# Optimization experiments

Measured on AMD Instinct MI355X. Metric: run time of the kernel, lower is better.

## Reference

```python
import jax, jax.numpy as jnp
import numpy as np

EMBED_DIM = 2048
NUM_HEADS = 16
HEAD_DIM = EMBED_DIM // NUM_HEADS
ROPE_BASE = 10000.0


def _rope_cos_sin(seq_len, head_dim, dtype):
    # half-split (LLaMA-style) rotary embedding tables, shape [S, D]
    inv_freq = 1.0 / (ROPE_BASE ** (jnp.arange(0, head_dim, 2, dtype=jnp.float32) / head_dim))
    ang = jnp.arange(seq_len, dtype=jnp.float32)[:, None] * inv_freq[None, :]  # [S, D/2]
    cos = jnp.concatenate([jnp.cos(ang), jnp.cos(ang)], axis=-1).astype(dtype)
    sin = jnp.concatenate([jnp.sin(ang), jnp.sin(ang)], axis=-1).astype(dtype)
    return cos, sin


def _rotate_half(t):
    d = t.shape[-1] // 2
    return jnp.concatenate([-t[..., d:], t[..., :d]], axis=-1)


def setup_inputs() -> dict:
    key = jax.random.key(0)
    ks = jax.random.split(key, 9)
    B, S, E = 2, 2048, EMBED_DIM
    sc = 1.0 / np.sqrt(E)
    return {
        "x": jax.random.normal(ks[0], (B, S, E), jnp.float32),
        "Wq": jax.random.normal(ks[1], (E, E), jnp.float32) * sc,
        "bq": jax.random.normal(ks[2], (E,), jnp.float32) * 0.01,
        "Wk": jax.random.normal(ks[3], (E, E), jnp.float32) * sc,
        "bk": jax.random.normal(ks[4], (E,), jnp.float32) * 0.01,
        "Wv": jax.random.normal(ks[5], (E, E), jnp.float32) * sc,
        "bv": jax.random.normal(ks[6], (E,), jnp.float32) * 0.01,
        "Wo": jax.random.normal(ks[7], (E, E), jnp.float32) * sc,
        "bo": jax.random.normal(ks[8], (E,), jnp.float32) * 0.01,
    }


def reference(x, Wq, bq, Wk, bk, Wv, bv, Wo, bo):
    B, S, E = x.shape
    H, D = NUM_HEADS, HEAD_DIM

    def split_heads(t):  # [B,S,E] -> [B,H,S,D]
        return t.reshape(B, S, H, D).transpose(0, 2, 1, 3)

    # torch nn.Linear: y = x @ W^T + b
    q = split_heads(x @ Wq.T + bq)
    k = split_heads(x @ Wk.T + bk)
    v = split_heads(x @ Wv.T + bv)

    cos, sin = _rope_cos_sin(S, D, x.dtype)  # [S, D]
    q = q * cos + _rotate_half(q) * sin
    k = k * cos + _rotate_half(k) * sin

    scale = 1.0 / jnp.sqrt(jnp.asarray(D, x.dtype))
    scores = jnp.einsum("bhsd,bhtd->bhst", q, k) * scale  # [B,H,S,S]
    attn = jax.nn.softmax(scores, axis=-1)
    ctx = jnp.einsum("bhst,bhtd->bhsd", attn, v)  # [B,H,S,D]
    ctx = ctx.transpose(0, 2, 1, 3).reshape(B, S, E)
    return ctx @ Wo.T + bo
```

## Files before the change

kernel.cpp:

```cpp
#include <hip/hip_runtime.h>
#include <stdint.h>

typedef unsigned short u16;
typedef unsigned int u32;
typedef __bf16 bf16x8 __attribute__((ext_vector_type(8)));
typedef u16 u16x8 __attribute__((ext_vector_type(8)));
typedef float f32x4 __attribute__((ext_vector_type(4)));
typedef float f32x16 __attribute__((ext_vector_type(16)));

#define NB 2
#define NS 2048
#define NE 2048
#define NH 16
#define ND 128
#define NM (NB*NS)

__device__ __forceinline__ float bf2f(u16 u){
  union { unsigned u; float f; } v; v.u = ((unsigned)u) << 16; return v.f;
}
__device__ __forceinline__ u16 f2bf(float f){
  union { float f; unsigned u; } v; v.f = f;
  unsigned r = v.u + 0x7fffu + ((v.u >> 16) & 1u);
  return (u16)(r >> 16);
}
__device__ __forceinline__ void gl_lds16(const u16* g, u16* l){
  __builtin_amdgcn_global_load_lds((const __attribute__((address_space(1))) unsigned int*)g,
                                   (__attribute__((address_space(3))) unsigned int*)l, 16, 0, 0);
}

__global__ __launch_bounds__(256) void k_cvt(const float* __restrict__ in, u16* __restrict__ out, int n4){
  int i = blockIdx.x * 256 + threadIdx.x;
  int stride = gridDim.x * 256;
  for (; i < n4; i += stride){
    float4 v = ((const float4*)in)[i];
    ushort4 o;
    o.x = f2bf(v.x); o.y = f2bf(v.y); o.z = f2bf(v.z); o.w = f2bf(v.w);
    ((ushort4*)out)[i] = o;
  }
}

__global__ __launch_bounds__(256) void k_cvt4(const float* __restrict__ w0, const float* __restrict__ w1,
                                              const float* __restrict__ w2, const float* __restrict__ w3,
                                              u16* __restrict__ o0, u16* __restrict__ o1,
                                              u16* __restrict__ o2, u16* __restrict__ o3){
  const int n4 = NE * NE / 4;
  int i = blockIdx.x * 256 + threadIdx.x;
  int stride = gridDim.x * 256;
  for (; i < 4 * n4; i += stride){
    int seg = i >> 20;
    int off = i & (n4 - 1);
    const float* in = seg == 0 ? w0 : seg == 1 ? w1 : seg == 2 ? w2 : w3;
    u16*        out = seg == 0 ? o0 : seg == 1 ? o1 : seg == 2 ? o2 : o3;
    float4 v = ((const float4*)in)[off];
    ushort4 o;
    o.x = f2bf(v.x); o.y = f2bf(v.y); o.z = f2bf(v.z); o.w = f2bf(v.w);
    ((ushort4*)out)[off] = o;
  }
}

__global__ __launch_bounds__(256) void k_tables(float* __restrict__ cosT, float* __restrict__ sinT){
  int idx = blockIdx.x * 256 + threadIdx.x;
  int s = idx >> 6, i = idx & 63;
  float inv = exp2f(-(float)(2 * i) * (13.287712379549449f / 128.0f));
  float ang = (float)s * inv;
  float c = cosf(ang), sn = sinf(ang);
  cosT[s * ND + i]      = c;  cosT[s * ND + 64 + i] = c;
  sinT[s * ND + i]      = sn; sinT[s * ND + 64 + i] = sn;
}

template<int MODE>
__global__ __launch_bounds__(512, 2) void k_gemm(const u16* __restrict__ A, const u16* __restrict__ W,
                                                 const float* __restrict__ bias,
                                                 const float* __restrict__ cosT, const float* __restrict__ sinT,
                                                 float qs, void* __restrict__ outp)
{
  __shared__ __align__(16) u16 lds[49152];
  const int t    = threadIdx.x;
  const int lane = t & 63;
  const int g    = lane >> 4;
  const int q    = lane & 15;
  const int wid  = t >> 6;
  const int wr   = (wid >> 1) * 64;
  const int wc   = (wid & 1) * 64;

  const int bid = blockIdx.x;
  const int v   = (bid & 7) * 32 + (bid >> 3);
  const int bm  = (v >> 4) * 256;
  const int bn  = (v & 15) * 128;

  int aoff[4], aldso[4], boff[2], bldso[2];
  #pragma unroll
  for (int c = 0; c < 4; ++c){
    int o = c * 8192 + t * 16;
    int row = o >> 7;
    int cb = (o & 127) ^ ((row & 7) << 4);
    aldso[c] = o >> 1;
    aoff[c]  = row * NE + (cb >> 1);
  }
  #pragma unroll
  for (int c = 0; c < 2; ++c){
    int o = c * 8192 + t * 16;
    int row = o >> 7;
    int cb = (o & 127) ^ ((row & 7) << 4);
    bldso[c] = o >> 1;
    boff[c]  = row * NE + (cb >> 1);
  }
  const u16* Abase = A + (size_t)bm * NE;
  const u16* Wbase = W + (size_t)bn * NE;

  int ard[2][4], brd[2][4];
  #pragma unroll
  for (int kk = 0; kk < 2; ++kk){
    #pragma unroll
    for (int m = 0; m < 4; ++m){
      int row = wr + m * 16 + q;
      ard[kk][m] = row * 128 + ((kk * 64 + g * 16) ^ ((row & 7) << 4));
    }
    #pragma unroll
    for (int n = 0; n < 4; ++n){
      int row = wc + n * 16 + q;
      brd[kk][n] = row * 128 + ((kk * 64 + g * 16) ^ ((row & 7) << 4));
    }
  }

  #pragma unroll
  for (int c = 0; c < 4; ++c) gl_lds16(Abase + aoff[c], lds + aldso[c]);
  #pragma unroll
  for (int c = 0; c < 2; ++c) gl_lds16(Wbase + boff[c], lds + 16384 + bldso[c]);

  f32x4 acc[4][4] = {};

  for (int kt = 0; kt < 32; ++kt){
    const int cbb = (kt & 1) ? 24576 : 0;
    if (kt < 31){
      const int sbb = cbb ^ 24576;
      const int go  = (kt + 1) * 64;
      #pragma unroll
      for (int c = 0; c < 4; ++c) gl_lds16(Abase + go + aoff[c], lds + sbb + aldso[c]);
      #pragma unroll
      for (int c = 0; c < 2; ++c) gl_lds16(Wbase + go + boff[c], lds + sbb + 16384 + bldso[c]);
      asm volatile("s_waitcnt vmcnt(6)" ::: "memory");
    } else {
      asm volatile("s_waitcnt vmcnt(0)" ::: "memory");
    }
    __builtin_amdgcn_s_barrier();

    const char* Ap = (const char*)(lds + cbb);
    const char* Bp = (const char*)(lds + cbb + 16384);

    {
      bf16x8 af[4], bfr[4];
      #pragma unroll
      for (int m = 0; m < 4; ++m) af[m]  = *(const bf16x8*)(Ap + ard[0][m]);
      #pragma unroll
      for (int n = 0; n < 4; ++n) bfr[n] = *(const bf16x8*)(Bp + brd[0][n]);
      __builtin_amdgcn_s_setprio(1);
      #pragma unroll
      for (int m = 0; m < 4; ++m)
        #pragma unroll
        for (int n = 0; n < 4; ++n)
          acc[m][n] = __builtin_amdgcn_mfma_f32_16x16x32_bf16(af[m], bfr[n], acc[m][n], 0, 0, 0);
      __builtin_amdgcn_s_setprio(0);
    }
    __builtin_amdgcn_s_barrier();

    {
      bf16x8 af[4], bfr[4];
      #pragma unroll
      for (int m = 0; m < 4; ++m) af[m]  = *(const bf16x8*)(Ap + ard[1][m]);
      #pragma unroll
      for (int n = 0; n < 4; ++n) bfr[n] = *(const bf16x8*)(Bp + brd[1][n]);
      __builtin_amdgcn_s_setprio(1);
      #pragma unroll
      for (int m = 0; m < 4; ++m)
        #pragma unroll
        for (int n = 0; n < 4; ++n)
          acc[m][n] = __builtin_amdgcn_mfma_f32_16x16x32_bf16(af[m], bfr[n], acc[m][n], 0, 0, 0);
      __builtin_amdgcn_s_setprio(0);
    }
    __builtin_amdgcn_s_barrier();
  }

  if constexpr (MODE == 2){
    float* out = (float*)outp;
    #pragma unroll
    for (int m = 0; m < 4; ++m)
      #pragma unroll
      for (int n = 0; n < 4; ++n){
        int col = bn + wc + n * 16 + q;
        float bv = bias[col];
        #pragma unroll
        for (int j = 0; j < 4; ++j){
          int row = bm + wr + m * 16 + g * 4 + j;
          out[(size_t)row * NE + col] = acc[m][n][j] + bv;
        }
      }
  } else if constexpr (MODE == 1){
    u16* out = (u16*)outp;
    __syncthreads();
    #pragma unroll
    for (int m = 0; m < 4; ++m)
      #pragma unroll
      for (int n = 0; n < 4; ++n){
        int d = wc + n * 16 + q;
        float bv = bias[bn + d];
        #pragma unroll
        for (int j = 0; j < 4; ++j){
          int sl = wr + m * 16 + g * 4 + j;
          lds[d * 264 + sl] = f2bf(acc[m][n][j] + bv);
        }
      }
    __syncthreads();
    const int b = bm >> 11, h = bn >> 7, sbase = bm & 2047;
    const int dq = t >> 4;
    const int sq = (t & 15) * 16;
    #pragma unroll
    for (int rep = 0; rep < 4; ++rep){
      int d = rep * 32 + dq;
      const u16* src = lds + d * 264 + sq;
      u16* dp = out + ((size_t)((b * NH + h) * ND + d)) * NS + sbase + sq;
      *(u16x8*)(dp)     = *(const u16x8*)(src);
      *(u16x8*)(dp + 8) = *(const u16x8*)(src + 8);
    }
  } else {
    u16* out = (u16*)outp;
    __syncthreads();
    #pragma unroll
    for (int m = 0; m < 4; ++m)
      #pragma unroll
      for (int n = 0; n < 4; ++n){
        int cl = wc + n * 16 + q;
        float bv = bias[bn + cl];
        #pragma unroll
        for (int j = 0; j < 4; ++j){
          int rl = wr + m * 16 + g * 4 + j;
          lds[rl * 132 + cl] = f2bf(acc[m][n][j] + bv);
        }
      }
    __syncthreads();
    #pragma unroll
    for (int m = 0; m < 4; ++m)
      #pragma unroll
      for (int n = 0; n < 4; ++n){
        int cl  = wc + n * 16 + q;
        int col = bn + cl;
        int h = col >> 7;
        float bv = bias[col];
        #pragma unroll
        for (int j = 0; j < 4; ++j){
          int rl = wr + m * 16 + g * 4 + j;
          int row = bm + rl;
          int b = row >> 11, s = row & 2047;
          float mine    = acc[m][n][j] + bv;
          float partner = bf2f(lds[rl * 132 + (cl ^ 64)]);
          float rot = (cl < 64) ? -partner : partner;
          float val = (mine * cosT[s * ND + cl] + rot * sinT[s * ND + cl]) * qs;
          out[(((size_t)(b * NH + h)) * NS + s) * ND + cl] = f2bf(val);
        }
      }
  }
}

template<bool D1>
__device__ __forceinline__ void pswap(u32 &a, u32 &b){
  if constexpr (D1) asm volatile("v_permlane32_swap_b32 %0, %1" : "+v"(a), "+v"(b));
  else              asm volatile("v_permlane32_swap_b32 %0, %1" : "+v"(b), "+v"(a));
}

#define AT_BODY(KT, SCC, SCN, KSTG, VSTG, KNXT, VCUR, SK, SV, VM, LAST)               \
  {                                                                                   \
    if (SK){ const int kb = ((KT) + 2) * 64 * ND;                                     \
      _Pragma("unroll") for (int c = 0; c < 4; ++c)                                   \
        gl_lds16(Kbase + kb + koff[c], (KSTG) + kldso[c]); }                          \
    if (SV){ const int vb = ((KT) + 1) * 64;                                          \
      _Pragma("unroll") for (int c = 0; c < 4; ++c)                                   \
        gl_lds16(Vbase + vb + voff[c], (VSTG) + vldso[c]); }                          \
    asm volatile("s_waitcnt vmcnt(" VM ")" ::: "memory");                             \
    __builtin_amdgcn_s_barrier();                                                     \
    float tA[8];                                                                      \
    _Pragma("unroll") for (int i = 0; i < 8; ++i)                                     \
      tA[i] = fmaxf(fmaxf(SCC[0][2*i], SCC[0][2*i+1]), fmaxf(SCC[1][2*i], SCC[1][2*i+1])); \
    float pmax = fmaxf(fmaxf(fmaxf(tA[0],tA[1]), fmaxf(tA[2],tA[3])),                 \
                       fmaxf(fmaxf(tA[4],tA[5]), fmaxf(tA[6],tA[7])));                \
    if (!(LAST)){                                                                     \
      SCN[0] = (f32x16)(0.f); SCN[1] = (f32x16)(0.f);                                 \
      __builtin_amdgcn_s_setprio(1);                                                  \
      _Pragma("unroll") for (int kk = 0; kk < 8; ++kk){                               \
        bf16x8 kf = *(const bf16x8*)((KNXT) + krd[0][kk]);                            \
        SCN[0] = __builtin_amdgcn_mfma_f32_32x32x16_bf16(kf, qf[kk], SCN[0], 0, 0, 0);\
      }                                                                               \
      __builtin_amdgcn_s_setprio(0);                                                  \
    }                                                                                 \
    pmax = fmaxf(pmax, __shfl_xor(pmax, 32));                                         \
    if (__any(pmax > mrow + 8.0f)){                                                   \
      float nm = fmaxf(mrow, pmax);                                                   \
      float rs = exp2f(mrow - nm);                                                    \
      lrow *= rs;                                                                     \
      _Pragma("unroll") for (int dt = 0; dt < 4; ++dt)                                \
        _Pragma("unroll") for (int r = 0; r < 16; ++r) acc[dt][r] *= rs;              \
      mrow = nm;                                                                      \
    }                                                                                 \
    float ts = 0.f;                                                                   \
    _Pragma("unroll") for (int r = 0; r < 16; ++r){                                   \
      float e = exp2f(SCC[0][r] - mrow); SCC[0][r] = e; ts += e; }                    \
    if (!(LAST)){                                                                     \
      __builtin_amdgcn_s_setprio(1);                                                  \
      _Pragma("unroll") for (int kk = 0; kk < 8; ++kk){                               \
        bf16x8 kf = *(const bf16x8*)((KNXT) + krd[1][kk]);                            \
        SCN[1] = __builtin_amdgcn_mfma_f32_32x32x16_bf16(kf, qf[kk], SCN[1], 0, 0, 0);\
      }                                                                               \
      __builtin_amdgcn_s_setprio(0);                                                  \
    }                                                                                 \
    _Pragma("unroll") for (int r = 0; r < 16; ++r){                                   \
      float e = exp2f(SCC[1][r] - mrow); SCC[1][r] = e; ts += e; }                    \
    ts += __shfl_xor(ts, 32);                                                         \
    lrow += ts;                                                                       \
    __builtin_amdgcn_s_setprio(1);                                                    \
    _Pragma("unroll") for (int t2 = 0; t2 < 2; ++t2)                                  \
      _Pragma("unroll") for (int kk2 = 0; kk2 < 2; ++kk2){                            \
        u32 a0, a1, b0, b1;                                                           \
        asm("v_cvt_pk_bf16_f32 %0, %1, %2" : "=v"(a0) : "v"(SCC[t2][8*kk2+0]), "v"(SCC[t2][8*kk2+1])); \
        asm("v_cvt_pk_bf16_f32 %0, %1, %2" : "=v"(a1) : "v"(SCC[t2][8*kk2+2]), "v"(SCC[t2][8*kk2+3])); \
        asm("v_cvt_pk_bf16_f32 %0, %1, %2" : "=v"(b0) : "v"(SCC[t2][8*kk2+4]), "v"(SCC[t2][8*kk2+5])); \
        asm("v_cvt_pk_bf16_f32 %0, %1, %2" : "=v"(b1) : "v"(SCC[t2][8*kk2+6]), "v"(SCC[t2][8*kk2+7])); \
        pswap<D1>(a0, b0); pswap<D1>(a1, b1);                                         \
        union { u32 u[4]; bf16x8 v; } pf;                                             \
        pf.u[0] = a0; pf.u[1] = a1; pf.u[2] = b0; pf.u[3] = b1;                       \
        const int kkf = 2*t2 + kk2;                                                   \
        _Pragma("unroll") for (int dt = 0; dt < 4; ++dt){                             \
          bf16x8 vf = *(const bf16x8*)((VCUR) + vrd[kkf][dt]);                        \
          acc[dt] = __builtin_amdgcn_mfma_f32_32x32x16_bf16(vf, pf.v, acc[dt], 0, 0, 0); \
        }                                                                             \
      }                                                                               \
    __builtin_amdgcn_s_setprio(0);                                                    \
    if (!(LAST)) __builtin_amdgcn_s_barrier();                                        \
  }

template<bool D1>
__device__ __forceinline__ void attn_impl(const u16* __restrict__ Qa, const u16* __restrict__ Ka,
                                          const u16* __restrict__ Vt, u16* __restrict__ ctx,
                                          u16* Ks0, u16* Ks1, u16* Vs0, u16* Vs1)
{
  const int t    = threadIdx.x;
  const int lane = t & 63;
  const int w    = t >> 6;
  const int l31  = lane & 31;
  const int hi   = lane >> 5;

  const int v   = (blockIdx.x & 7) * 64 + (blockIdx.x >> 3);
  const int qb  = v & 15;
  const int bh  = v >> 4;
  const int q0  = qb * 128 + w * 32;

  int koff[4], kldso[4], voff[4], vldso[4];
  #pragma unroll
  for (int c = 0; c < 4; ++c){
    int o = c * 4096 + t * 16;
    { int row = o >> 8, col = o & 255; int cs = col ^ ((row & 15) << 4);
      kldso[c] = o >> 1;  koff[c] = row * ND + (cs >> 1); }
    { int row = o >> 7, col = o & 127; int cs = col ^ ((row & 7) << 4);
      vldso[c] = o >> 1;  voff[c] = row * NS + (cs >> 1); }
  }
  const u16* Kbase = Ka + (size_t)bh * NS * ND;
  const u16* Vbase = Vt + (size_t)bh * ND * NS;

  bf16x8 qf[8];
  #pragma unroll
  for (int kk = 0; kk < 8; ++kk)
    qf[kk] = *(const bf16x8*)(Qa + ((size_t)bh * NS + q0 + l31) * ND + kk * 16 + hi * 8);

  #pragma unroll
  for (int c = 0; c < 4; ++c) gl_lds16(Kbase + koff[c], Ks0 + kldso[c]);
  #pragma unroll
  for (int c = 0; c < 4; ++c) gl_lds16(Vbase + voff[c], Vs0 + vldso[c]);
  #pragma unroll
  for (int c = 0; c < 4; ++c) gl_lds16(Kbase + 64 * ND + koff[c], Ks1 + kldso[c]);

  int krd[2][8], vrd[4][4];
  #pragma unroll
  for (int t2 = 0; t2 < 2; ++t2){
    const int row = t2 * 32 + l31, sw = (row & 15) << 4;
    #pragma unroll
    for (int kk = 0; kk < 8; ++kk)
      krd[t2][kk] = row * 256 + ((kk * 32 + hi * 16) ^ sw);
  }
  #pragma unroll
  for (int dt = 0; dt < 4; ++dt){
    const int row = dt * 32 + l31, sw = (row & 7) << 4;
    #pragma unroll
    for (int kk = 0; kk < 4; ++kk)
      vrd[kk][dt] = row * 128 + ((kk * 32 + hi * 16) ^ sw);
  }

  asm volatile("s_waitcnt vmcnt(8)" ::: "memory");
  __builtin_amdgcn_s_barrier();

  f32x16 scA[2], scB[2];
  scA[0] = (f32x16)(0.f); scA[1] = (f32x16)(0.f);
  {
    const char* Kl = (const char*)Ks0;
    #pragma unroll
    for (int t2 = 0; t2 < 2; ++t2)
      #pragma unroll
      for (int kk = 0; kk < 8; ++kk){
        bf16x8 kf = *(const bf16x8*)(Kl + krd[t2][kk]);
        scA[t2] = __builtin_amdgcn_mfma_f32_32x32x16_bf16(kf, qf[kk], scA[t2], 0, 0, 0);
      }
  }
  __builtin_amdgcn_s_barrier();

  f32x16 acc[4] = {};
  float mrow = -3e38f, lrow = 0.f;

  for (int kt = 0; kt < 30; kt += 2){
    AT_BODY(kt,     scA, scB, Ks0, Vs1, (const char*)Ks1, (const char*)Vs0, 1, 1, "8", 0);
    AT_BODY(kt + 1, scB, scA, Ks1, Vs0, (const char*)Ks0, (const char*)Vs1, 1, 1, "8", 0);
  }
  AT_BODY(30, scA, scB, Ks0, Vs1, (const char*)Ks1, (const char*)Vs0, 0, 1, "4", 0);
  AT_BODY(31, scB, scA, Ks1, Vs0, (const char*)Ks0, (const char*)Vs1, 0, 0, "0", 1);

  const float inv = 1.0f / lrow;
  const int b = bh >> 4, h = bh & 15;
  const int s = q0 + l31;
  #pragma unroll
  for (int dt = 0; dt < 4; ++dt)
    #pragma unroll
    for (int a2 = 0; a2 < 4; ++a2){
      const int d0 = dt * 32 + 8 * a2 + 4 * hi;
      ushort4 o;
      o.x = f2bf(acc[dt][4*a2+0] * inv);
      o.y = f2bf(acc[dt][4*a2+1] * inv);
      o.z = f2bf(acc[dt][4*a2+2] * inv);
      o.w = f2bf(acc[dt][4*a2+3] * inv);
      *(ushort4*)(ctx + ((size_t)(b * NS + s)) * NE + h * ND + d0) = o;
    }
}

__global__ __launch_bounds__(256, 2) void k_attn(const u16* __restrict__ Qa, const u16* __restrict__ Ka,
                                                 const u16* __restrict__ Vt, u16* __restrict__ ctx)
{
  __shared__ __align__(16) u16 Ks[2][64 * 128];
  __shared__ __align__(16) u16 Vs[2][128 * 64];
  const int lane = threadIdx.x & 63;
  u32 xx = (u32)lane, yy = 64u + (u32)lane;
  asm volatile("v_permlane32_swap_b32 %0, %1" : "+v"(xx), "+v"(yy));
  const bool isD1 = (xx == (u32)(lane < 32 ? lane : lane + 32));
  if (isD1) attn_impl<true >(Qa, Ka, Vt, ctx, &Ks[0][0], &Ks[1][0], &Vs[0][0], &Vs[1][0]);
  else      attn_impl<false>(Qa, Ka, Vt, ctx, &Ks[0][0], &Ks[1][0], &Vs[0][0], &Vs[1][0]);
}

extern "C" void kernel_launch(void* const* d_in, const int* in_sizes, int n_in,
                              void* d_out, int out_size, void* d_ws, size_t ws_size,
                              hipStream_t stream)
{
  const float* x  = (const float*)d_in[0];
  const float* Wq = (const float*)d_in[1];
  const float* bq = (const float*)d_in[2];
  const float* Wk = (const float*)d_in[3];
  const float* bk = (const float*)d_in[4];
  const float* Wv = (const float*)d_in[5];
  const float* bv = (const float*)d_in[6];
  const float* Wo = (const float*)d_in[7];
  const float* bo = (const float*)d_in[8];

  char* ws = (char*)d_ws;
  u16*   xbf  = (u16*)(ws);
  u16*   wqb  = (u16*)(ws + 16777216);
  u16*   wkb  = (u16*)(ws + 25165824);
  u16*   wvb  = (u16*)(ws + 33554432);
  u16*   wob  = (u16*)(ws + 41943040);
  float* cosT = (float*)(ws + 50331648);
  float* sinT = (float*)(ws + 51380224);
  u16*   Qa   = (u16*)(ws + 52428800);
  u16*   Ka   = (u16*)(ws + 69206016);
  u16*   Vt   = (u16*)(ws + 85983232);
  u16*   ctx  = xbf;

  const float sl = 0.08838834764831845f * 1.4426950408889634f;

  k_cvt<<<1024, 256, 0, stream>>>(x, xbf, NM * NE / 4);
  k_cvt4<<<2048, 256, 0, stream>>>(Wq, Wk, Wv, Wo, wqb, wkb, wvb, wob);
  k_tables<<<NS * 64 / 256, 256, 0, stream>>>(cosT, sinT);

  k_gemm<0><<<256, 512, 0, stream>>>(xbf, wqb, bq, cosT, sinT, sl,   (void*)Qa);
  k_gemm<0><<<256, 512, 0, stream>>>(xbf, wkb, bk, cosT, sinT, 1.0f, (void*)Ka);
  k_gemm<1><<<256, 512, 0, stream>>>(xbf, wvb, bv, nullptr, nullptr, 1.0f, (void*)Vt);

  k_attn<<<512, 256, 0, stream>>>(Qa, Ka, Vt, ctx);

  k_gemm<2><<<256, 512, 0, stream>>>(ctx, wob, bo, nullptr, nullptr, 1.0f, d_out);
}
```

Measured before the change: 278.4 us.

## Load V fragments directly from global into registers, drop V LDS staging

The attention kernel no longer stages V tiles through double-buffered shared memory. Each wave loads its V fragments straight from global memory into registers at the start of each KV step and waits on them just before the PV MFMAs, with the vmcnt counts and barriers reworked to match. This halves LDS use (which may allow higher occupancy) and removes LDS reads and writes for V, at the cost of more VGPRs and redundant global or L2 traffic, since each wave fetches V separately. The GEMM inner loop is also folded into a two-iteration loop, which drops one barrier between the two k-halves.

```diff
diff --git a/kernel.cpp b/kernel.cpp
--- a/kernel.cpp
+++ b/kernel.cpp
@@ -148,28 +148,13 @@
     const char* Ap = (const char*)(lds + cbb);
     const char* Bp = (const char*)(lds + cbb + 16384);
 
-    {
+    #pragma unroll
+    for (int kk = 0; kk < 2; ++kk){
       bf16x8 af[4], bfr[4];
       #pragma unroll
-      for (int m = 0; m < 4; ++m) af[m]  = *(const bf16x8*)(Ap + ard[0][m]);
-      #pragma unroll
-      for (int n = 0; n < 4; ++n) bfr[n] = *(const bf16x8*)(Bp + brd[0][n]);
-      __builtin_amdgcn_s_setprio(1);
-      #pragma unroll
-      for (int m = 0; m < 4; ++m)
-        #pragma unroll
-        for (int n = 0; n < 4; ++n)
-          acc[m][n] = __builtin_amdgcn_mfma_f32_16x16x32_bf16(af[m], bfr[n], acc[m][n], 0, 0, 0);
-      __builtin_amdgcn_s_setprio(0);
-    }
-    __builtin_amdgcn_s_barrier();
-
-    {
-      bf16x8 af[4], bfr[4];
-      #pragma unroll
-      for (int m = 0; m < 4; ++m) af[m]  = *(const bf16x8*)(Ap + ard[1][m]);
-      #pragma unroll
-      for (int n = 0; n < 4; ++n) bfr[n] = *(const bf16x8*)(Bp + brd[1][n]);
+      for (int m = 0; m < 4; ++m) af[m]  = *(const bf16x8*)(Ap + ard[kk][m]);
+      #pragma unroll
+      for (int n = 0; n < 4; ++n) bfr[n] = *(const bf16x8*)(Bp + brd[kk][n]);
       __builtin_amdgcn_s_setprio(1);
       #pragma unroll
       for (int m = 0; m < 4; ++m)
@@ -267,23 +252,25 @@
   else              asm volatile("v_permlane32_swap_b32 %0, %1" : "+v"(b), "+v"(a));
 }
 
-#define AT_BODY(KT, SCC, SCN, KSTG, VSTG, KNXT, VCUR, SK, SV, VM, LAST)               \
+#define AT_BODY(KT, SCC, SCN, KSTG, KNXT, SK, SQK, VMTOP, VMPV)                       \
   {                                                                                   \
+    bf16x8 vf[4][4];                                                                  \
+    { const int vb = (KT) * 64;                                                       \
+      _Pragma("unroll") for (int dt = 0; dt < 4; ++dt)                                \
+        _Pragma("unroll") for (int kkf = 0; kkf < 4; ++kkf)                           \
+          vf[kkf][dt] = *(const bf16x8*)(Vrow + dt * (32 * NS) + vb + kkf * 16); }    \
     if (SK){ const int kb = ((KT) + 2) * 64 * ND;                                     \
       _Pragma("unroll") for (int c = 0; c < 4; ++c)                                   \
         gl_lds16(Kbase + kb + koff[c], (KSTG) + kldso[c]); }                          \
-    if (SV){ const int vb = ((KT) + 1) * 64;                                          \
-      _Pragma("unroll") for (int c = 0; c < 4; ++c)                                   \
-        gl_lds16(Vbase + vb + voff[c], (VSTG) + vldso[c]); }                          \
-    asm volatile("s_waitcnt vmcnt(" VM ")" ::: "memory");                             \
+    asm volatile("s_waitcnt vmcnt(" VMTOP ")" ::: "memory");                          \
     __builtin_amdgcn_s_barrier();                                                     \
     float tA[8];                                                                      \
     _Pragma("unroll") for (int i = 0; i < 8; ++i)                                     \
       tA[i] = fmaxf(fmaxf(SCC[0][2*i], SCC[0][2*i+1]), fmaxf(SCC[1][2*i], SCC[1][2*i+1])); \
     float pmax = fmaxf(fmaxf(fmaxf(tA[0],tA[1]), fmaxf(tA[2],tA[3])),                 \
                        fmaxf(fmaxf(tA[4],tA[5]), fmaxf(tA[6],tA[7])));                \
-    if (!(LAST)){                                                                     \
-      SCN[0] = (f32x16)(0.f); SCN[1] = (f32x16)(0.f);                                 \
+    if (SQK){                                                                         \
+      SCN[0] = (f32x16)(0.f);                                                         \
       __builtin_amdgcn_s_setprio(1);                                                  \
       _Pragma("unroll") for (int kk = 0; kk < 8; ++kk){                               \
         bf16x8 kf = *(const bf16x8*)((KNXT) + krd[0][kk]);                            \
@@ -303,18 +290,21 @@
     float ts = 0.f;                                                                   \
     _Pragma("unroll") for (int r = 0; r < 16; ++r){                                   \
       float e = exp2f(SCC[0][r] - mrow); SCC[0][r] = e; ts += e; }                    \
-    if (!(LAST)){                                                                     \
+    if (SQK){                                                                         \
+      SCN[1] = (f32x16)(0.f);                                                         \
       __builtin_amdgcn_s_setprio(1);                                                  \
       _Pragma("unroll") for (int kk = 0; kk < 8; ++kk){                               \
         bf16x8 kf = *(const bf16x8*)((KNXT) + krd[1][kk]);                            \
         SCN[1] = __builtin_amdgcn_mfma_f32_32x32x16_bf16(kf, qf[kk], SCN[1], 0, 0, 0);\
       }                                                                               \
       __builtin_amdgcn_s_setprio(0);                                                  \
+      __builtin_amdgcn_s_barrier();     \
     }                                                                                 \
     _Pragma("unroll") for (int r = 0; r < 16; ++r){                                   \
       float e = exp2f(SCC[1][r] - mrow); SCC[1][r] = e; ts += e; }                    \
     ts += __shfl_xor(ts, 32);                                                         \
     lrow += ts;                                                                       \
+    asm volatile("s_waitcnt vmcnt(" VMPV ")" ::: "memory");                           \
     __builtin_amdgcn_s_setprio(1);                                                    \
     _Pragma("unroll") for (int t2 = 0; t2 < 2; ++t2)                                  \
       _Pragma("unroll") for (int kk2 = 0; kk2 < 2; ++kk2){                            \
@@ -327,19 +317,16 @@
         union { u32 u[4]; bf16x8 v; } pf;                                             \
         pf.u[0] = a0; pf.u[1] = a1; pf.u[2] = b0; pf.u[3] = b1;                       \
         const int kkf = 2*t2 + kk2;                                                   \
-        _Pragma("unroll") for (int dt = 0; dt < 4; ++dt){                             \
-          bf16x8 vf = *(const bf16x8*)((VCUR) + vrd[kkf][dt]);                        \
-          acc[dt] = __builtin_amdgcn_mfma_f32_32x32x16_bf16(vf, pf.v, acc[dt], 0, 0, 0); \
-        }                                                                             \
+        _Pragma("unroll") for (int dt = 0; dt < 4; ++dt)                              \
+          acc[dt] = __builtin_amdgcn_mfma_f32_32x32x16_bf16(vf[kkf][dt], pf.v, acc[dt], 0, 0, 0); \
       }                                                                               \
     __builtin_amdgcn_s_setprio(0);                                                    \
-    if (!(LAST)) __builtin_amdgcn_s_barrier();                                        \
   }
 
 template<bool D1>
 __device__ __forceinline__ void attn_impl(const u16* __restrict__ Qa, const u16* __restrict__ Ka,
                                           const u16* __restrict__ Vt, u16* __restrict__ ctx,
-                                          u16* Ks0, u16* Ks1, u16* Vs0, u16* Vs1)
+                                          u16* Ks0, u16* Ks1)
 {
   const int t    = threadIdx.x;
   const int lane = t & 63;
@@ -352,31 +339,26 @@
   const int bh  = v >> 4;
   const int q0  = qb * 128 + w * 32;
 
-  int koff[4], kldso[4], voff[4], vldso[4];
+  int koff[4], kldso[4];
   #pragma unroll
   for (int c = 0; c < 4; ++c){
     int o = c * 4096 + t * 16;
-    { int row = o >> 8, col = o & 255; int cs = col ^ ((row & 15) << 4);
-      kldso[c] = o >> 1;  koff[c] = row * ND + (cs >> 1); }
-    { int row = o >> 7, col = o & 127; int cs = col ^ ((row & 7) << 4);
-      vldso[c] = o >> 1;  voff[c] = row * NS + (cs >> 1); }
+    int row = o >> 8, col = o & 255; int cs = col ^ ((row & 15) << 4);
+    kldso[c] = o >> 1;  koff[c] = row * ND + (cs >> 1);
   }
   const u16* Kbase = Ka + (size_t)bh * NS * ND;
-  const u16* Vbase = Vt + (size_t)bh * ND * NS;
+  const u16* Vrow  = Vt + (size_t)bh * ND * NS + (size_t)l31 * NS + hi * 8;
 
   bf16x8 qf[8];
   #pragma unroll
   for (int kk = 0; kk < 8; ++kk)
     qf[kk] = *(const bf16x8*)(Qa + ((size_t)bh * NS + q0 + l31) * ND + kk * 16 + hi * 8);
-
   #pragma unroll
   for (int c = 0; c < 4; ++c) gl_lds16(Kbase + koff[c], Ks0 + kldso[c]);
   #pragma unroll
-  for (int c = 0; c < 4; ++c) gl_lds16(Vbase + voff[c], Vs0 + vldso[c]);
-  #pragma unroll
   for (int c = 0; c < 4; ++c) gl_lds16(Kbase + 64 * ND + koff[c], Ks1 + kldso[c]);
 
-  int krd[2][8], vrd[4][4];
+  int krd[2][8];
   #pragma unroll
   for (int t2 = 0; t2 < 2; ++t2){
     const int row = t2 * 32 + l31, sw = (row & 15) << 4;
@@ -384,15 +366,8 @@
     for (int kk = 0; kk < 8; ++kk)
       krd[t2][kk] = row * 256 + ((kk * 32 + hi * 16) ^ sw);
   }
-  #pragma unroll
-  for (int dt = 0; dt < 4; ++dt){
-    const int row = dt * 32 + l31, sw = (row & 7) << 4;
-    #pragma unroll
-    for (int kk = 0; kk < 4; ++kk)
-      vrd[kk][dt] = row * 128 + ((kk * 32 + hi * 16) ^ sw);
-  }
-
-  asm volatile("s_waitcnt vmcnt(8)" ::: "memory");
+
+  asm volatile("s_waitcnt vmcnt(4)" ::: "memory");
   __builtin_amdgcn_s_barrier();
 
   f32x16 scA[2], scB[2];
@@ -413,11 +388,11 @@
   float mrow = -3e38f, lrow = 0.f;
 
   for (int kt = 0; kt < 30; kt += 2){
-    AT_BODY(kt,     scA, scB, Ks0, Vs1, (const char*)Ks1, (const char*)Vs0, 1, 1, "8", 0);
-    AT_BODY(kt + 1, scB, scA, Ks1, Vs0, (const char*)Ks0, (const char*)Vs1, 1, 1, "8", 0);
-  }
-  AT_BODY(30, scA, scB, Ks0, Vs1, (const char*)Ks1, (const char*)Vs0, 0, 1, "4", 0);
-  AT_BODY(31, scB, scA, Ks1, Vs0, (const char*)Ks0, (const char*)Vs1, 0, 0, "0", 1);
+    AT_BODY(kt,     scA, scB, Ks0, (const char*)Ks1, 1, 1, "20", "4");
+    AT_BODY(kt + 1, scB, scA, Ks1, (const char*)Ks0, 1, 1, "20", "4");
+  }
+  AT_BODY(30, scA, scB, Ks0, (const char*)Ks1, 0, 1, "16", "0");
+  AT_BODY(31, scB, scA, Ks1, (const char*)Ks0, 0, 0, "16", "0");
 
   const float inv = 1.0f / lrow;
   const int b = bh >> 4, h = bh & 15;
@@ -440,13 +415,12 @@
                                                  const u16* __restrict__ Vt, u16* __restrict__ ctx)
 {
   __shared__ __align__(16) u16 Ks[2][64 * 128];
-  __shared__ __align__(16) u16 Vs[2][128 * 64];
   const int lane = threadIdx.x & 63;
   u32 xx = (u32)lane, yy = 64u + (u32)lane;
   asm volatile("v_permlane32_swap_b32 %0, %1" : "+v"(xx), "+v"(yy));
   const bool isD1 = (xx == (u32)(lane < 32 ? lane : lane + 32));
-  if (isD1) attn_impl<true >(Qa, Ka, Vt, ctx, &Ks[0][0], &Ks[1][0], &Vs[0][0], &Vs[1][0]);
-  else      attn_impl<false>(Qa, Ka, Vt, ctx, &Ks[0][0], &Ks[1][0], &Vs[0][0], &Vs[1][0]);
+  if (isD1) attn_impl<true >(Qa, Ka, Vt, ctx, &Ks[0][0], &Ks[1][0]);
+  else      attn_impl<false>(Qa, Ka, Vt, ctx, &Ks[0][0], &Ks[1][0]);
 }
 
 extern "C" void kernel_launch(void* const* d_in, const int* in_sizes, int n_in,
```

New measurement: 447.9 us. 1.61x slower.

## Pack two attention tiles per 512-thread block with staggered ping-pong scheduling

Applied to the files above, without the earlier changes.

The attention kernel now launches 256 blocks of 512 threads, and each block holds two independent 256-thread groups that work on separate query tiles with their own K/V LDS buffers. One group is offset by an extra barrier at the start and the other gets a matching barrier at the end, so the groups' softmax and MFMA phases interleave through shared s_barriers. Inside the loop body the V tile load is issued after the first barrier, and a second waitcnt plus barrier is placed before the PV MFMAs, splitting each iteration into two synchronisation phases. The GEMM's two half-iteration blocks are folded into an unrolled loop, which drops one of the three barriers per k-step. The barriers now couple both groups, so any imbalance between them stalls the whole block.

```diff
diff --git a/kernel.cpp b/kernel.cpp
--- a/kernel.cpp
+++ b/kernel.cpp
@@ -148,28 +148,13 @@
     const char* Ap = (const char*)(lds + cbb);
     const char* Bp = (const char*)(lds + cbb + 16384);
 
-    {
+    #pragma unroll
+    for (int kk = 0; kk < 2; ++kk){
       bf16x8 af[4], bfr[4];
       #pragma unroll
-      for (int m = 0; m < 4; ++m) af[m]  = *(const bf16x8*)(Ap + ard[0][m]);
-      #pragma unroll
-      for (int n = 0; n < 4; ++n) bfr[n] = *(const bf16x8*)(Bp + brd[0][n]);
-      __builtin_amdgcn_s_setprio(1);
-      #pragma unroll
-      for (int m = 0; m < 4; ++m)
-        #pragma unroll
-        for (int n = 0; n < 4; ++n)
-          acc[m][n] = __builtin_amdgcn_mfma_f32_16x16x32_bf16(af[m], bfr[n], acc[m][n], 0, 0, 0);
-      __builtin_amdgcn_s_setprio(0);
-    }
-    __builtin_amdgcn_s_barrier();
-
-    {
-      bf16x8 af[4], bfr[4];
-      #pragma unroll
-      for (int m = 0; m < 4; ++m) af[m]  = *(const bf16x8*)(Ap + ard[1][m]);
-      #pragma unroll
-      for (int n = 0; n < 4; ++n) bfr[n] = *(const bf16x8*)(Bp + brd[1][n]);
+      for (int m = 0; m < 4; ++m) af[m]  = *(const bf16x8*)(Ap + ard[kk][m]);
+      #pragma unroll
+      for (int n = 0; n < 4; ++n) bfr[n] = *(const bf16x8*)(Bp + brd[kk][n]);
       __builtin_amdgcn_s_setprio(1);
       #pragma unroll
       for (int m = 0; m < 4; ++m)
@@ -267,30 +252,16 @@
   else              asm volatile("v_permlane32_swap_b32 %0, %1" : "+v"(b), "+v"(a));
 }
 
-#define AT_BODY(KT, SCC, SCN, KSTG, VSTG, KNXT, VCUR, SK, SV, VM, LAST)               \
+#define AT_BODY(KT, SCC, SCN, KSTG, VSTG, KNXT, VCUR, SK, SV, SQK, VM1, VM2)          \
   {                                                                                   \
     if (SK){ const int kb = ((KT) + 2) * 64 * ND;                                     \
       _Pragma("unroll") for (int c = 0; c < 4; ++c)                                   \
         gl_lds16(Kbase + kb + koff[c], (KSTG) + kldso[c]); }                          \
-    if (SV){ const int vb = ((KT) + 1) * 64;                                          \
-      _Pragma("unroll") for (int c = 0; c < 4; ++c)                                   \
-        gl_lds16(Vbase + vb + voff[c], (VSTG) + vldso[c]); }                          \
-    asm volatile("s_waitcnt vmcnt(" VM ")" ::: "memory");                             \
-    __builtin_amdgcn_s_barrier();                                                     \
     float tA[8];                                                                      \
     _Pragma("unroll") for (int i = 0; i < 8; ++i)                                     \
       tA[i] = fmaxf(fmaxf(SCC[0][2*i], SCC[0][2*i+1]), fmaxf(SCC[1][2*i], SCC[1][2*i+1])); \
     float pmax = fmaxf(fmaxf(fmaxf(tA[0],tA[1]), fmaxf(tA[2],tA[3])),                 \
                        fmaxf(fmaxf(tA[4],tA[5]), fmaxf(tA[6],tA[7])));                \
-    if (!(LAST)){                                                                     \
-      SCN[0] = (f32x16)(0.f); SCN[1] = (f32x16)(0.f);                                 \
-      __builtin_amdgcn_s_setprio(1);                                                  \
-      _Pragma("unroll") for (int kk = 0; kk < 8; ++kk){                               \
-        bf16x8 kf = *(const bf16x8*)((KNXT) + krd[0][kk]);                            \
-        SCN[0] = __builtin_amdgcn_mfma_f32_32x32x16_bf16(kf, qf[kk], SCN[0], 0, 0, 0);\
-      }                                                                               \
-      __builtin_amdgcn_s_setprio(0);                                                  \
-    }                                                                                 \
     pmax = fmaxf(pmax, __shfl_xor(pmax, 32));                                         \
     if (__any(pmax > mrow + 8.0f)){                                                   \
       float nm = fmaxf(mrow, pmax);                                                   \
@@ -300,10 +271,25 @@
         _Pragma("unroll") for (int r = 0; r < 16; ++r) acc[dt][r] *= rs;              \
       mrow = nm;                                                                      \
     }                                                                                 \
+    asm volatile("s_waitcnt vmcnt(" VM1 ")" ::: "memory");                            \
+    __builtin_amdgcn_s_barrier();                                                     \
+    if (SV){ const int vb = ((KT) + 1) * 64;                                          \
+      _Pragma("unroll") for (int c = 0; c < 4; ++c)                                   \
+        gl_lds16(Vbase + vb + voff[c], (VSTG) + vldso[c]); }                          \
     float ts = 0.f;                                                                   \
+    if (SQK){                                                                         \
+      SCN[0] = (f32x16)(0.f);                                                         \
+      __builtin_amdgcn_s_setprio(1);                                                  \
+      _Pragma("unroll") for (int kk = 0; kk < 8; ++kk){                               \
+        bf16x8 kf = *(const bf16x8*)((KNXT) + krd[0][kk]);                            \
+        SCN[0] = __builtin_amdgcn_mfma_f32_32x32x16_bf16(kf, qf[kk], SCN[0], 0, 0, 0);\
+      }                                                                               \
+      __builtin_amdgcn_s_setprio(0);                                                  \
+    }                                                                                 \
     _Pragma("unroll") for (int r = 0; r < 16; ++r){                                   \
       float e = exp2f(SCC[0][r] - mrow); SCC[0][r] = e; ts += e; }                    \
-    if (!(LAST)){                                                                     \
+    if (SQK){                                                                         \
+      SCN[1] = (f32x16)(0.f);                                                         \
       __builtin_amdgcn_s_setprio(1);                                                  \
       _Pragma("unroll") for (int kk = 0; kk < 8; ++kk){                               \
         bf16x8 kf = *(const bf16x8*)((KNXT) + krd[1][kk]);                            \
@@ -315,6 +301,8 @@
       float e = exp2f(SCC[1][r] - mrow); SCC[1][r] = e; ts += e; }                    \
     ts += __shfl_xor(ts, 32);                                                         \
     lrow += ts;                                                                       \
+    asm volatile("s_waitcnt vmcnt(" VM2 ")" ::: "memory");                            \
+    __builtin_amdgcn_s_barrier();                                                     \
     __builtin_amdgcn_s_setprio(1);                                                    \
     _Pragma("unroll") for (int t2 = 0; t2 < 2; ++t2)                                  \
       _Pragma("unroll") for (int kk2 = 0; kk2 < 2; ++kk2){                            \
@@ -333,29 +321,30 @@
         }                                                                             \
       }                                                                               \
     __builtin_amdgcn_s_setprio(0);                                                    \
-    if (!(LAST)) __builtin_amdgcn_s_barrier();                                        \
   }
 
 template<bool D1>
 __device__ __forceinline__ void attn_impl(const u16* __restrict__ Qa, const u16* __restrict__ Ka,
                                           const u16* __restrict__ Vt, u16* __restrict__ ctx,
-                                          u16* Ks0, u16* Ks1, u16* Vs0, u16* Vs1)
+                                          u16* Ks0, u16* Ks1, u16* Vs0, u16* Vs1, int grp)
 {
   const int t    = threadIdx.x;
+  const int tg   = t & 255;
   const int lane = t & 63;
-  const int w    = t >> 6;
+  const int w    = (t >> 6) & 3;
   const int l31  = lane & 31;
   const int hi   = lane >> 5;
 
-  const int v   = (blockIdx.x & 7) * 64 + (blockIdx.x >> 3);
-  const int qb  = v & 15;
-  const int bh  = v >> 4;
-  const int q0  = qb * 128 + w * 32;
+  const int v    = (blockIdx.x & 7) * 32 + (blockIdx.x >> 3);
+  const int unit = (v << 1) | grp;
+  const int qb   = unit & 15;
+  const int bh   = unit >> 4;
+  const int q0   = qb * 128 + w * 32;
 
   int koff[4], kldso[4], voff[4], vldso[4];
   #pragma unroll
   for (int c = 0; c < 4; ++c){
-    int o = c * 4096 + t * 16;
+    int o = c * 4096 + tg * 16;
     { int row = o >> 8, col = o & 255; int cs = col ^ ((row & 15) << 4);
       kldso[c] = o >> 1;  koff[c] = row * ND + (cs >> 1); }
     { int row = o >> 7, col = o & 127; int cs = col ^ ((row & 7) << 4);
@@ -364,15 +353,14 @@
   const u16* Kbase = Ka + (size_t)bh * NS * ND;
   const u16* Vbase = Vt + (size_t)bh * ND * NS;
 
+  if (grp) __builtin_amdgcn_s_barrier();
+
   bf16x8 qf[8];
   #pragma unroll
   for (int kk = 0; kk < 8; ++kk)
     qf[kk] = *(const bf16x8*)(Qa + ((size_t)bh * NS + q0 + l31) * ND + kk * 16 + hi * 8);
-
   #pragma unroll
   for (int c = 0; c < 4; ++c) gl_lds16(Kbase + koff[c], Ks0 + kldso[c]);
-  #pragma unroll
-  for (int c = 0; c < 4; ++c) gl_lds16(Vbase + voff[c], Vs0 + vldso[c]);
   #pragma unroll
   for (int c = 0; c < 4; ++c) gl_lds16(Kbase + 64 * ND + koff[c], Ks1 + kldso[c]);
 
@@ -392,8 +380,11 @@
       vrd[kk][dt] = row * 128 + ((kk * 32 + hi * 16) ^ sw);
   }
 
-  asm volatile("s_waitcnt vmcnt(8)" ::: "memory");
+  asm volatile("s_waitcnt vmcnt(4)" ::: "memory");
   __builtin_amdgcn_s_barrier();
+
+  #pragma unroll
+  for (int c = 0; c < 4; ++c) gl_lds16(Vbase + voff[c], Vs0 + vldso[c]);
 
   f32x16 scA[2], scB[2];
   scA[0] = (f32x16)(0.f); scA[1] = (f32x16)(0.f);
@@ -413,11 +404,13 @@
   float mrow = -3e38f, lrow = 0.f;
 
   for (int kt = 0; kt < 30; kt += 2){
-    AT_BODY(kt,     scA, scB, Ks0, Vs1, (const char*)Ks1, (const char*)Vs0, 1, 1, "8", 0);
-    AT_BODY(kt + 1, scB, scA, Ks1, Vs0, (const char*)Ks0, (const char*)Vs1, 1, 1, "8", 0);
-  }
-  AT_BODY(30, scA, scB, Ks0, Vs1, (const char*)Ks1, (const char*)Vs0, 0, 1, "4", 0);
-  AT_BODY(31, scB, scA, Ks1, Vs0, (const char*)Ks0, (const char*)Vs1, 0, 0, "0", 1);
+    AT_BODY(kt,     scA, scB, Ks0, Vs1, (const char*)Ks1, (const char*)Vs0, 1, 1, 1, "8", "8");
+    AT_BODY(kt + 1, scB, scA, Ks1, Vs0, (const char*)Ks0, (const char*)Vs1, 1, 1, 1, "8", "8");
+  }
+  AT_BODY(30, scA, scB, Ks0, Vs1, (const char*)Ks1, (const char*)Vs0, 0, 1, 1, "4", "4");
+  AT_BODY(31, scB, scA, Ks1, Vs0, (const char*)Ks0, (const char*)Vs1, 0, 0, 0, "4", "0");
+
+  if (!grp) __builtin_amdgcn_s_barrier();
 
   const float inv = 1.0f / lrow;
   const int b = bh >> 4, h = bh & 15;
@@ -436,17 +429,18 @@
     }
 }
 
-__global__ __launch_bounds__(256, 2) void k_attn(const u16* __restrict__ Qa, const u16* __restrict__ Ka,
+__global__ __launch_bounds__(512, 1) void k_attn(const u16* __restrict__ Qa, const u16* __restrict__ Ka,
                                                  const u16* __restrict__ Vt, u16* __restrict__ ctx)
 {
-  __shared__ __align__(16) u16 Ks[2][64 * 128];
-  __shared__ __align__(16) u16 Vs[2][128 * 64];
+  __shared__ __align__(16) u16 Ks[2][2][64 * 128];
+  __shared__ __align__(16) u16 Vs[2][2][128 * 64];
+  const int grp = threadIdx.x >> 8;
   const int lane = threadIdx.x & 63;
   u32 xx = (u32)lane, yy = 64u + (u32)lane;
   asm volatile("v_permlane32_swap_b32 %0, %1" : "+v"(xx), "+v"(yy));
   const bool isD1 = (xx == (u32)(lane < 32 ? lane : lane + 32));
-  if (isD1) attn_impl<true >(Qa, Ka, Vt, ctx, &Ks[0][0], &Ks[1][0], &Vs[0][0], &Vs[1][0]);
-  else      attn_impl<false>(Qa, Ka, Vt, ctx, &Ks[0][0], &Ks[1][0], &Vs[0][0], &Vs[1][0]);
+  if (isD1) attn_impl<true >(Qa, Ka, Vt, ctx, &Ks[grp][0][0], &Ks[grp][1][0], &Vs[grp][0][0], &Vs[grp][1][0], grp);
+  else      attn_impl<false>(Qa, Ka, Vt, ctx, &Ks[grp][0][0], &Ks[grp][1][0], &Vs[grp][0][0], &Vs[grp][1][0], grp);
 }
 
 extern "C" void kernel_launch(void* const* d_in, const int* in_sizes, int n_in,
@@ -486,7 +480,7 @@
   k_gemm<0><<<256, 512, 0, stream>>>(xbf, wkb, bk, cosT, sinT, 1.0f, (void*)Ka);
   k_gemm<1><<<256, 512, 0, stream>>>(xbf, wvb, bv, nullptr, nullptr, 1.0f, (void*)Vt);
 
-  k_attn<<<512, 256, 0, stream>>>(Qa, Ka, Vt, ctx);
+  k_attn<<<256, 512, 0, stream>>>(Qa, Ka, Vt, ctx);
 
   k_gemm<2><<<256, 512, 0, stream>>>(ctx, wob, bo, nullptr, nullptr, 1.0f, d_out);
 }
```

Result: no change. 275.8 us (-0.9%).
